# Performance work log

Measured on AMD Instinct MI355X. Metric: run time of the kernel, lower is better.

The kernel has to match this reference:

```python
import jax, jax.numpy as jnp
import numpy as np

B, S, D = 32, 2048, 1024
TEMP = 9.0  # RelaxedBernoulli temperature (torch.tensor([9]))


def setup_inputs() -> dict:
    key = jax.random.key(0)
    ks = jax.random.split(key, 12)
    sd = 1.0 / np.sqrt(D)
    sd2 = 1.0 / np.sqrt(2 * D)
    return {
        "h_t": jax.random.normal(ks[0], (B, D), jnp.float32),
        "h_s": jax.random.normal(ks[1], (B, S, D), jnp.float32),
        "auxi_hs": jax.random.normal(ks[2], (B, S, D), jnp.float32),
        "noise_u": jax.random.uniform(ks[3], (B, S, 1), jnp.float32),
        # linear_map: Linear(2*dim, 1) with bias
        "Wmap": jax.random.normal(ks[4], (2 * D,), jnp.float32) * sd2,
        "bmap": jax.random.normal(ks[5], (), jnp.float32) * sd2,
        # mlp_h: Linear(dim, dim) + Tanh + Linear(dim, 1)
        "W1": jax.random.normal(ks[6], (D, D), jnp.float32) * sd,
        "b1": jax.random.normal(ks[7], (D,), jnp.float32) * sd,
        "W2": jax.random.normal(ks[8], (D,), jnp.float32) * sd,
        "b2": jax.random.normal(ks[9], (), jnp.float32) * sd,
        # linear_out: Linear(2*dim, dim, bias=False) (attn_type='dot')
        "Wout": jax.random.normal(ks[10], (D, 2 * D), jnp.float32) * sd2,
    }


def reference(h_t, h_s, auxi_hs, noise_u, Wmap, bmap, W1, b1, W2, b2, Wout):
    # h_t: (B, D) one-step query; h_s, auxi_hs: (B, S, D)
    d = h_s.shape[-1]
    # linear_map(concat(auxi_hs, H_t)) without materializing the (B,S,2D) concat
    Wm_a, Wm_t = Wmap[:d], Wmap[d:]
    logits_p = jnp.einsum('bsd,d->bs', auxi_hs, Wm_a) + (h_t @ Wm_t)[:, None] + bmap  # (B,S)
    logits_p = logits_p[..., None]  # (B,S,1); note logit(sigmoid(x)) == x
    # RelaxedBernoulli(temp=9, probs=sigmoid(logits_p)).sample() with explicit uniform noise
    eps = 1e-7
    u = jnp.clip(noise_u, eps, 1.0 - eps)
    logistic = jnp.log(u) - jnp.log1p(-u)  # (B,S,1)
    G = jax.nn.sigmoid((logits_p + logistic) / TEMP)  # (B,S,1)
    # mlp_h(h_s): Linear -> tanh -> Linear
    e = jnp.einsum('bsd,d->bs', jnp.tanh(jnp.einsum('bsd,ed->bse', h_s, W1) + b1), W2) + b2
    e = e[..., None]  # (B,S,1)
    # custom softmax: max over dim 0 (batch!), exp, gate
    v = jnp.max(e, axis=0, keepdims=True)  # (1,S,1)
    scores = jnp.exp(e - v) * G  # (B,S,1)
    align = scores[..., 0] / jnp.sum(scores[..., 0], axis=1, keepdims=True)  # (B,S)
    c = jnp.einsum('bs,bsd->bd', align, h_s)  # (B,D)
    attn_h = jnp.tanh(jnp.concatenate([c, h_t], axis=-1) @ Wout.T)  # (B,D)
    return attn_h, align
```

## Files before the change

### kernel.cpp

```cpp
#include <hip/hip_runtime.h>
#include <hip/hip_bf16.h>
#include <math.h>

#define B_ 32
#define S_ 2048
#define D_ 1024
#define TEMP_ 9.0f

typedef __attribute__((ext_vector_type(8))) short short8;
typedef __attribute__((ext_vector_type(4))) float f32x4;
typedef __attribute__((ext_vector_type(4))) unsigned short ushort4v;

__device__ __forceinline__ unsigned short f2b(float f) {
  union { float f; unsigned int u; } v; v.f = f;
  unsigned int r = v.u;
  r += 0x7fffu + ((r >> 16) & 1u);
  return (unsigned short)(r >> 16);
}
__device__ __forceinline__ float b2f(unsigned short b) {
  union { float f; unsigned int u; } v; v.u = ((unsigned int)b) << 16;
  return v.f;
}
__device__ __forceinline__ float tanh_fast(float x) {
  float ez = __expf(2.f * x);
  return 1.f - __fdividef(2.f, ez + 1.f);
}

#define GLOAD_LDS16(g, l) \
  __builtin_amdgcn_global_load_lds((const __attribute__((address_space(1))) void*)(g), \
                                   (__attribute__((address_space(3))) void*)(l), 16, 0, 0)

__global__ void k_conv(const float* __restrict__ src, unsigned short* __restrict__ dst, int n8) {
  int i = blockIdx.x * 256 + threadIdx.x;
  if (i >= n8) return;
  const float4* g = reinterpret_cast<const float4*>(src) + (size_t)i * 2;
  float4 x0 = g[0], x1 = g[1];
  uint4 w;
  w.x = f2b(x0.x) | ((unsigned)f2b(x0.y) << 16);
  w.y = f2b(x0.z) | ((unsigned)f2b(x0.w) << 16);
  w.z = f2b(x1.x) | ((unsigned)f2b(x1.y) << 16);
  w.w = f2b(x1.z) | ((unsigned)f2b(x1.w) << 16);
  reinterpret_cast<uint4*>(dst)[i] = w;
}

__global__ void k_pack_w1(const float* __restrict__ W1, unsigned short* __restrict__ w1t) {
  int c = blockIdx.x * 256 + threadIdx.x;
  int l  = c & 63;
  int kt = (c >> 6) & 31;
  int cg = c >> 11;
  int col = cg * 16 + (l & 15);
  int k0  = kt * 32 + (l >> 4) * 8;
  const float* src = W1 + (size_t)col * D_ + k0;
  float4 x0 = *reinterpret_cast<const float4*>(src);
  float4 x1 = *reinterpret_cast<const float4*>(src + 4);
  uint4 w;
  w.x = f2b(x0.x) | ((unsigned)f2b(x0.y) << 16);
  w.y = f2b(x0.z) | ((unsigned)f2b(x0.w) << 16);
  w.z = f2b(x1.x) | ((unsigned)f2b(x1.y) << 16);
  w.w = f2b(x1.z) | ((unsigned)f2b(x1.w) << 16);
  reinterpret_cast<uint4*>(w1t)[c] = w;
}

__global__ void k0_tdot(const float* __restrict__ h_t, const float* __restrict__ Wmap,
                        const float* __restrict__ bmap, float* __restrict__ tdot) {
  int b = blockIdx.x;
  int t = threadIdx.x;
  float p = 0.f;
  for (int k = t; k < D_; k += 256) p += h_t[b*D_ + k] * Wmap[D_ + k];
  __shared__ float red[256];
  red[t] = p; __syncthreads();
  for (int off = 128; off > 0; off >>= 1) { if (t < off) red[t] += red[t+off]; __syncthreads(); }
  if (t == 0) tdot[b] = red[0] + bmap[0];
}

__global__ void k1_gate(const float* __restrict__ aux, const float* __restrict__ Wmap,
                        const float* __restrict__ noise, const float* __restrict__ tdot,
                        float* __restrict__ Gout) {
  int w = (blockIdx.x * 256 + threadIdx.x) >> 6;
  int lane = threadIdx.x & 63;
  const float4* arow = reinterpret_cast<const float4*>(aux + (size_t)w * D_);
  const float4* wrow = reinterpret_cast<const float4*>(Wmap);
  float p = 0.f;
  for (int it = 0; it < 4; ++it) {
    float4 a = arow[it*64 + lane];
    float4 m = wrow[it*64 + lane];
    p += a.x*m.x + a.y*m.y + a.z*m.z + a.w*m.w;
  }
  for (int msk = 32; msk > 0; msk >>= 1) p += __shfl_xor(p, msk);
  if (lane == 0) {
    int b = w >> 11;
    float logits = p + tdot[b];
    float u = noise[w];
    u = fminf(fmaxf(u, 1e-7f), 1.f - 1e-7f);
    float logistic = logf(u) - log1pf(-u);
    float x = (logits + logistic) / TEMP_;
    Gout[w] = 1.f / (1.f + expf(-x));
  }
}

extern __shared__ unsigned short lds2[];

__global__ __launch_bounds__(256, 2) void k2gt(
    const unsigned short* __restrict__ Ag, const unsigned short* __restrict__ w1t,
    const float* __restrict__ b1, const float* __restrict__ W2,
    float* __restrict__ e_buf,
    const float* __restrict__ aux, const float* __restrict__ Wmap,
    const float* __restrict__ noise, const float* __restrict__ tdot,
    float* __restrict__ Gout) {
  int bid = blockIdx.x;
  int xcd = bid & 7;
  int sub = bid >> 3;
  int cc  = sub & 3;
  int rc  = xcd + 8 * (sub >> 2);
  int rowBase = rc * 128;
  int colBase = cc * 256;

  int t = threadIdx.x;
  int lane = t & 63;
  int wv = t >> 6;
  int kslot = lane >> 4;

  int aOff[8];
#pragma unroll
  for (int m = 0; m < 8; ++m) {
    int r = m * 16 + (lane & 15);
    aOff[m] = r * 64 + ((kslot ^ ((r >> 1) & 3)) << 4);
  }

  const unsigned short* gA[2];
  int dstA[2];
#pragma unroll
  for (int i = 0; i < 2; ++i) {
    int c = i * 256 + t;
    int r = c >> 2;
    int clog = (c & 3) ^ ((r >> 1) & 3);
    gA[i] = Ag + (size_t)(rowBase + r) * D_ + clog * 8;
    dstA[i] = c * 16;
  }

  const unsigned short* pB[4];
#pragma unroll
  for (int n = 0; n < 4; ++n) {
    int cg = (colBase >> 4) + wv * 4 + n;
    pB[n] = w1t + (size_t)cg * 16384 + lane * 8;
  }

  f32x4 acc[8][4] = {};
  short8 bfA[4], bfB[4];

#define STAGE(TT) do {                                                         \
    char* _ba = (char*)lds2 + ((TT) & 3) * 8192;                               \
    GLOAD_LDS16(gA[0] + (TT) * 32, _ba + dstA[0]);                             \
    GLOAD_LDS16(gA[1] + (TT) * 32, _ba + dstA[1]);                             \
  } while (0)

#define K2_TILE(T, VM, DO_B, DO_S, BFC, BFN) do {                              \
    asm volatile("s_waitcnt lgkmcnt(0)\n\ts_waitcnt vmcnt(" #VM ")" ::: "memory"); \
    __builtin_amdgcn_s_barrier();                                              \
    const char* _ab = (const char*)lds2 + ((T) & 3) * 8192;                    \
    short8 af[8];                                                              \
    _Pragma("unroll")                                                          \
    for (int m = 0; m < 8; ++m)                                                \
      af[m] = *reinterpret_cast<const short8*>(_ab + aOff[m]);                 \
    if (DO_B) {                                                                \
      _Pragma("unroll")                                                        \
      for (int n = 0; n < 4; ++n)                                              \
        BFN[n] = *reinterpret_cast<const short8*>(pB[n] + ((T) + 1) * 512);    \
    }                                                                          \
    if (DO_S) STAGE((T) + 3);                                                  \
    __builtin_amdgcn_s_setprio(1);                                             \
    _Pragma("unroll")                                                          \
    for (int m = 0; m < 8; ++m)                                                \
      _Pragma("unroll")                                                        \
      for (int n = 0; n < 4; ++n)                                              \
        acc[m][n] = __builtin_amdgcn_mfma_f32_16x16x32_bf16(af[m], BFC[n], acc[m][n], 0, 0, 0); \
    __builtin_amdgcn_s_setprio(0);                                             \
  } while (0)

  STAGE(0); STAGE(1); STAGE(2);
#pragma unroll
  for (int n = 0; n < 4; ++n)
    bfA[n] = *reinterpret_cast<const short8*>(pB[n]);

  K2_TILE(0, 0, true, true, bfA, bfB);
  K2_TILE(1, 2, true, true, bfB, bfA);
#pragma unroll
  for (int tt = 2; tt < 28; tt += 2) {
    K2_TILE(tt,     2, true, true, bfA, bfB);
    K2_TILE(tt + 1, 2, true, true, bfB, bfA);
  }
  K2_TILE(28, 2, true,  true,  bfA, bfB);
  K2_TILE(29, 2, true,  false, bfB, bfA);
  K2_TILE(30, 0, true,  false, bfA, bfB);
  K2_TILE(31, 0, false, false, bfB, bfA);
#undef K2_TILE
#undef STAGE

  float b1v[4], w2v[4];
#pragma unroll
  for (int n = 0; n < 4; ++n) {
    int col = colBase + wv * 64 + n * 16 + (lane & 15);
    b1v[n] = b1[col];
    w2v[n] = W2[col];
  }
#pragma unroll
  for (int m = 0; m < 8; ++m) {
#pragma unroll
    for (int j = 0; j < 4; ++j) {
      float s = 0.f;
#pragma unroll
      for (int n = 0; n < 4; ++n)
        s += tanh_fast(acc[m][n][j] + b1v[n]) * w2v[n];
      s += __shfl_xor(s, 1);
      s += __shfl_xor(s, 2);
      s += __shfl_xor(s, 4);
      s += __shfl_xor(s, 8);
      if ((lane & 15) == 0) {
        int row = rowBase + m * 16 + ((lane >> 4) << 2) + j;
        atomicAdd(&e_buf[row], s);
      }
    }
  }

  {
    const float4* wrow = reinterpret_cast<const float4*>(Wmap);
    float4 m0 = wrow[lane], m1 = wrow[64 + lane], m2 = wrow[128 + lane], m3 = wrow[192 + lane];
    int rowG = (bid << 5) | (wv << 3);
#pragma unroll 2
    for (int i = 0; i < 8; ++i) {
      int row = rowG + i;
      const float4* arow = reinterpret_cast<const float4*>(aux + (size_t)row * D_);
      float4 a0 = arow[lane], a1 = arow[64 + lane], a2 = arow[128 + lane], a3 = arow[192 + lane];
      float p = a0.x*m0.x + a0.y*m0.y + a0.z*m0.z + a0.w*m0.w
              + a1.x*m1.x + a1.y*m1.y + a1.z*m1.z + a1.w*m1.w
              + a2.x*m2.x + a2.y*m2.y + a2.z*m2.z + a2.w*m2.w
              + a3.x*m3.x + a3.y*m3.y + a3.z*m3.z + a3.w*m3.w;
      for (int msk = 32; msk > 0; msk >>= 1) p += __shfl_xor(p, msk);
      if (lane == 0) {
        float logits = p + tdot[row >> 11];
        float u = noise[row];
        u = fminf(fmaxf(u, 1e-7f), 1.f - 1e-7f);
        float logistic = logf(u) - log1pf(-u);
        float x = (logits + logistic) / TEMP_;
        Gout[row] = 1.f / (1.f + expf(-x));
      }
    }
  }
}

#define BM 128
#define BN 128
#define BK 64
__global__ __launch_bounds__(256) void k2_egemm_f32(
    const float* __restrict__ h_s, const float* __restrict__ W1,
    const float* __restrict__ b1, const float* __restrict__ W2,
    float* __restrict__ e_buf) {
  __shared__ unsigned short As[BM * BK];
  __shared__ unsigned short Bs[BN * BK];
  int bid = blockIdx.x;
  int colBase = (bid & 7) * BN;
  int rowBase = (bid >> 3) * BM;
  int t = threadIdx.x;
  int lane = t & 63;
  int wave = t >> 6;
  int wr = wave >> 1, wc = wave & 1;
  f32x4 acc[4][4] = {};
  for (int k0 = 0; k0 < D_; k0 += BK) {
    __syncthreads();
    for (int i = 0; i < 4; ++i) {
      int flat = i*256 + t;
      int r = flat >> 3;
      int c8 = flat & 7;
      int byte = (r*128 + c8*16) ^ ((r & 7) << 4);
      {
        const float4* g = reinterpret_cast<const float4*>(h_s + (size_t)(rowBase + r)*D_ + k0 + c8*8);
        float4 x0 = g[0], x1 = g[1];
        uint4 w;
        w.x = f2b(x0.x) | ((unsigned)f2b(x0.y) << 16);
        w.y = f2b(x0.z) | ((unsigned)f2b(x0.w) << 16);
        w.z = f2b(x1.x) | ((unsigned)f2b(x1.y) << 16);
        w.w = f2b(x1.z) | ((unsigned)f2b(x1.w) << 16);
        *reinterpret_cast<uint4*>(reinterpret_cast<char*>(As) + byte) = w;
      }
      {
        const float4* g = reinterpret_cast<const float4*>(W1 + (size_t)(colBase + r)*D_ + k0 + c8*8);
        float4 x0 = g[0], x1 = g[1];
        uint4 w;
        w.x = f2b(x0.x) | ((unsigned)f2b(x0.y) << 16);
        w.y = f2b(x0.z) | ((unsigned)f2b(x0.w) << 16);
        w.z = f2b(x1.x) | ((unsigned)f2b(x1.y) << 16);
        w.w = f2b(x1.z) | ((unsigned)f2b(x1.w) << 16);
        *reinterpret_cast<uint4*>(reinterpret_cast<char*>(Bs) + byte) = w;
      }
    }
    __syncthreads();
    for (int kk = 0; kk < BK; kk += 32) {
      short8 af[4], bf[4];
      int kByte = kk*2 + ((lane >> 4) << 4);
      for (int m = 0; m < 4; ++m) {
        int r = wr*64 + m*16 + (lane & 15);
        int byte = (r*128 + kByte) ^ ((r & 7) << 4);
        af[m] = *reinterpret_cast<const short8*>(reinterpret_cast<const char*>(As) + byte);
      }
      for (int n = 0; n < 4; ++n) {
        int r = wc*64 + n*16 + (lane & 15);
        int byte = (r*128 + kByte) ^ ((r & 7) << 4);
        bf[n] = *reinterpret_cast<const short8*>(reinterpret_cast<const char*>(Bs) + byte);
      }
      for (int m = 0; m < 4; ++m)
        for (int n = 0; n < 4; ++n)
          acc[m][n] = __builtin_amdgcn_mfma_f32_16x16x32_bf16(af[m], bf[n], acc[m][n], 0, 0, 0);
    }
  }
  float b1v[4], w2v[4];
  for (int n = 0; n < 4; ++n) {
    int col = colBase + wc*64 + n*16 + (lane & 15);
    b1v[n] = b1[col];
    w2v[n] = W2[col];
  }
  for (int m = 0; m < 4; ++m) {
    for (int j = 0; j < 4; ++j) {
      float s = 0.f;
      for (int n = 0; n < 4; ++n)
        s += tanhf(acc[m][n][j] + b1v[n]) * w2v[n];
      s += __shfl_xor(s, 1);
      s += __shfl_xor(s, 2);
      s += __shfl_xor(s, 4);
      s += __shfl_xor(s, 8);
      if ((lane & 15) == 0) {
        int row = rowBase + wr*64 + m*16 + ((lane >> 4) << 2) + j;
        atomicAdd(&e_buf[row], s);
      }
    }
  }
}

__global__ void k3a_vmax(const float* __restrict__ e_buf, float* __restrict__ v) {
  int s = blockIdx.x * 256 + threadIdx.x;
  if (s >= S_) return;
  float m = -1e30f;
  for (int b = 0; b < B_; ++b) m = fmaxf(m, e_buf[b*S_ + s]);
  v[s] = m;
}

__global__ void k3b_align(const float* __restrict__ e_buf, const float* __restrict__ v,
                          float* __restrict__ galign) {
  int b = blockIdx.x;
  int t = threadIdx.x;
  __shared__ float sc[S_];
  __shared__ float red[256];
  float p = 0.f;
  for (int s = t; s < S_; s += 256) {
    float x = expf(e_buf[b*S_ + s] - v[s]) * galign[b*S_ + s];
    sc[s] = x;
    p += x;
  }
  red[t] = p; __syncthreads();
  for (int off = 128; off > 0; off >>= 1) { if (t < off) red[t] += red[t+off]; __syncthreads(); }
  float inv = 1.f / red[0];
  for (int s = t; s < S_; s += 256) galign[b*S_ + s] = sc[s] * inv;
}

__global__ void k4_ctx_bf16(const unsigned short* __restrict__ hsb, const float* __restrict__ align,
                            float* __restrict__ c) {
  int bid = blockIdx.x;
  int b = bid >> 6;
  int sBase = (bid & 63) * 32;
  int t = threadIdx.x;
  float4 accv = {0.f, 0.f, 0.f, 0.f};
  for (int si = 0; si < 32; ++si) {
    int s = sBase + si;
    float a = align[b*S_ + s];
    ushort4v hv = *reinterpret_cast<const ushort4v*>(hsb + (size_t)(b*S_ + s)*D_ + t*4);
    accv.x += a*b2f(hv.x); accv.y += a*b2f(hv.y); accv.z += a*b2f(hv.z); accv.w += a*b2f(hv.w);
  }
  atomicAdd(&c[b*D_ + t*4 + 0], accv.x);
  atomicAdd(&c[b*D_ + t*4 + 1], accv.y);
  atomicAdd(&c[b*D_ + t*4 + 2], accv.z);
  atomicAdd(&c[b*D_ + t*4 + 3], accv.w);
}

__global__ void k4_ctx_f32(const float* __restrict__ h_s, const float* __restrict__ align,
                           float* __restrict__ c) {
  int bid = blockIdx.x;
  int b = bid >> 6;
  int sBase = (bid & 63) * 32;
  int t = threadIdx.x;
  float4 accv = {0.f, 0.f, 0.f, 0.f};
  for (int si = 0; si < 32; ++si) {
    int s = sBase + si;
    float a = align[b*S_ + s];
    float4 hv = *reinterpret_cast<const float4*>(h_s + (size_t)(b*S_ + s)*D_ + t*4);
    accv.x += a*hv.x; accv.y += a*hv.y; accv.z += a*hv.z; accv.w += a*hv.w;
  }
  atomicAdd(&c[b*D_ + t*4 + 0], accv.x);
  atomicAdd(&c[b*D_ + t*4 + 1], accv.y);
  atomicAdd(&c[b*D_ + t*4 + 2], accv.z);
  atomicAdd(&c[b*D_ + t*4 + 3], accv.w);
}

__global__ void k5_out(const float* __restrict__ c, const float* __restrict__ h_t,
                       const float* __restrict__ Wout, float* __restrict__ out) {
  int W = (blockIdx.x * 256 + threadIdx.x) >> 6;
  int lane = threadIdx.x & 63;
  int b = W >> 10;
  int o = W & 1023;
  const float* wrow = Wout + (size_t)o * (2 * D_);
  float p = 0.f;
  for (int it = 0; it < 16; ++it) {
    int k = it*64 + lane;
    p += c[b*D_ + k] * wrow[k];
  }
  for (int it = 16; it < 32; ++it) {
    int k = it*64 + lane;
    p += h_t[b*D_ + (k - D_)] * wrow[k];
  }
  for (int m = 32; m > 0; m >>= 1) p += __shfl_xor(p, m);
  if (lane == 0) out[b*D_ + o] = tanhf(p);
}

extern "C" void kernel_launch(void* const* d_in, const int* in_sizes, int n_in,
                              void* d_out, int out_size, void* d_ws, size_t ws_size,
                              hipStream_t stream) {
  const float* h_t   = (const float*)d_in[0];
  const float* h_s   = (const float*)d_in[1];
  const float* aux   = (const float*)d_in[2];
  const float* noise = (const float*)d_in[3];
  const float* Wmap  = (const float*)d_in[4];
  const float* bmap  = (const float*)d_in[5];
  const float* W1    = (const float*)d_in[6];
  const float* b1    = (const float*)d_in[7];
  const float* W2    = (const float*)d_in[8];
  const float* Wout  = (const float*)d_in[10];

  float* out    = (float*)d_out;
  float* galign = out + B_*D_;

  const size_t HS_N   = (size_t)B_*S_*D_;
  const size_t W1_N   = (size_t)D_*D_;
  const size_t needed = HS_N*2 + W1_N*2 + (65536 + 32 + 2048 + 32768) * sizeof(float);

  if (ws_size >= needed) {
    unsigned short* hs_bf = (unsigned short*)d_ws;
    unsigned short* w1t   = hs_bf + HS_N;
    float* fws   = (float*)(w1t + W1_N);
    float* e_buf = fws;
    float* tdot  = fws + 65536;
    float* v     = fws + 65568;
    float* c     = fws + 67616;

    hipMemsetAsync(e_buf, 0, 65536 * sizeof(float), stream);
    hipMemsetAsync(c, 0, 32768 * sizeof(float), stream);

    hipFuncSetAttribute(reinterpret_cast<const void*>(k2gt),
                        hipFuncAttributeMaxDynamicSharedMemorySize, 32768);

    k_conv<<<(int)(HS_N/8/256), 256, 0, stream>>>(h_s, hs_bf, (int)(HS_N/8));
    k_pack_w1<<<512, 256, 0, stream>>>(W1, w1t);
    k0_tdot<<<32, 256, 0, stream>>>(h_t, Wmap, bmap, tdot);
    k2gt<<<2048, 256, 32768, stream>>>(hs_bf, w1t, b1, W2, e_buf,
                                       aux, Wmap, noise, tdot, galign);
    k3a_vmax<<<8, 256, 0, stream>>>(e_buf, v);
    k3b_align<<<32, 256, 0, stream>>>(e_buf, v, galign);
    k4_ctx_bf16<<<2048, 256, 0, stream>>>(hs_bf, galign, c);
    k5_out<<<8192, 256, 0, stream>>>(c, h_t, Wout, out);
  } else {
    float* ws    = (float*)d_ws;
    float* e_buf = ws;
    float* tdot  = ws + 65536;
    float* v     = ws + 65568;
    float* c     = ws + 67616;

    hipMemsetAsync(e_buf, 0, 65536 * sizeof(float), stream);
    hipMemsetAsync(c, 0, 32768 * sizeof(float), stream);

    k0_tdot<<<32, 256, 0, stream>>>(h_t, Wmap, bmap, tdot);
    k1_gate<<<16384, 256, 0, stream>>>(aux, Wmap, noise, tdot, galign);
    k2_egemm_f32<<<4096, 256, 0, stream>>>(h_s, W1, b1, W2, e_buf);
    k3a_vmax<<<8, 256, 0, stream>>>(e_buf, v);
    k3b_align<<<32, 256, 0, stream>>>(e_buf, v, galign);
    k4_ctx_f32<<<2048, 256, 0, stream>>>(h_s, galign, c);
    k5_out<<<8192, 256, 0, stream>>>(c, h_t, Wout, out);
  }
}
```

Measured before the change: 340.3 us.

## Remap GEMM warp tiling to 2x2 grid with 64x128 per-wave tiles

Changes the per-wave tile of the h_s·W1ᵀ MFMA GEMM from 128 rows × 64 cols to 64 rows × 128 cols, arranging the four waves as a 2×2 grid. The W1 packing kernel is reordered so each wave reads its eight B fragments for a k-step from one contiguous region. Each wave now issues half as many LDS reads for A and twice as many global loads for B per k-step. The aim is to cut LDS traffic and improve the balance of A versus B reuse, at the cost of more B register fragments and more global B bandwidth per wave.

```diff
diff --git a/kernel.cpp b/kernel.cpp
--- a/kernel.cpp
+++ b/kernel.cpp
@@ -44,12 +44,13 @@
 }
 
 __global__ void k_pack_w1(const float* __restrict__ W1, unsigned short* __restrict__ w1t) {
-  int c = blockIdx.x * 256 + threadIdx.x;
-  int l  = c & 63;
-  int kt = (c >> 6) & 31;
-  int cg = c >> 11;
-  int col = cg * 16 + (l & 15);
-  int k0  = kt * 32 + (l >> 4) * 8;
+  int c2 = blockIdx.x * 256 + threadIdx.x;
+  int l   = c2 & 63;
+  int n   = (c2 >> 6) & 7;
+  int T   = (c2 >> 9) & 31;
+  int rid = c2 >> 14;
+  int col = (rid >> 1) * 256 + (rid & 1) * 128 + n * 16 + (l & 15);
+  int k0  = T * 32 + (l >> 4) * 8;
   const float* src = W1 + (size_t)col * D_ + k0;
   float4 x0 = *reinterpret_cast<const float4*>(src);
   float4 x1 = *reinterpret_cast<const float4*>(src + 4);
@@ -58,7 +59,7 @@
   w.y = f2b(x0.z) | ((unsigned)f2b(x0.w) << 16);
   w.z = f2b(x1.x) | ((unsigned)f2b(x1.y) << 16);
   w.w = f2b(x1.z) | ((unsigned)f2b(x1.w) << 16);
-  reinterpret_cast<uint4*>(w1t)[c] = w;
+  reinterpret_cast<uint4*>(w1t)[c2] = w;
 }
 
 __global__ void k0_tdot(const float* __restrict__ h_t, const float* __restrict__ Wmap,
@@ -118,12 +119,13 @@
   int t = threadIdx.x;
   int lane = t & 63;
   int wv = t >> 6;
+  int wr = wv >> 1, wc = wv & 1;
   int kslot = lane >> 4;
 
-  int aOff[8];
-#pragma unroll
-  for (int m = 0; m < 8; ++m) {
-    int r = m * 16 + (lane & 15);
+  int aOff[4];
+#pragma unroll
+  for (int m = 0; m < 4; ++m) {
+    int r = wr * 64 + m * 16 + (lane & 15);
     aOff[m] = r * 64 + ((kslot ^ ((r >> 1) & 3)) << 4);
   }
 
@@ -138,15 +140,10 @@
     dstA[i] = c * 16;
   }
 
-  const unsigned short* pB[4];
-#pragma unroll
-  for (int n = 0; n < 4; ++n) {
-    int cg = (colBase >> 4) + wv * 4 + n;
-    pB[n] = w1t + (size_t)cg * 16384 + lane * 8;
-  }
-
-  f32x4 acc[8][4] = {};
-  short8 bfA[4], bfB[4];
+  const unsigned short* pBbase = w1t + (size_t)(cc * 2 + wc) * 131072 + lane * 8;
+
+  f32x4 acc[4][8] = {};
+  short8 bfA[8], bfB[8];
 
 #define STAGE(TT) do {                                                         \
     char* _ba = (char*)lds2 + ((TT) & 3) * 8192;                               \
@@ -158,65 +155,63 @@
     asm volatile("s_waitcnt lgkmcnt(0)\n\ts_waitcnt vmcnt(" #VM ")" ::: "memory"); \
     __builtin_amdgcn_s_barrier();                                              \
     const char* _ab = (const char*)lds2 + ((T) & 3) * 8192;                    \
-    short8 af[8];                                                              \
+    short8 af[4];                                                              \
     _Pragma("unroll")                                                          \
-    for (int m = 0; m < 8; ++m)                                                \
+    for (int m = 0; m < 4; ++m)                                                \
       af[m] = *reinterpret_cast<const short8*>(_ab + aOff[m]);                 \
     if (DO_B) {                                                                \
       _Pragma("unroll")                                                        \
-      for (int n = 0; n < 4; ++n)                                              \
-        BFN[n] = *reinterpret_cast<const short8*>(pB[n] + ((T) + 1) * 512);    \
+      for (int n = 0; n < 8; ++n)                                              \
+        BFN[n] = *reinterpret_cast<const short8*>(pBbase + ((T) + 1) * 4096 + n * 512); \
     }                                                                          \
     if (DO_S) STAGE((T) + 3);                                                  \
     __builtin_amdgcn_s_setprio(1);                                             \
     _Pragma("unroll")                                                          \
-    for (int m = 0; m < 8; ++m)                                                \
+    for (int m = 0; m < 4; ++m)                                                \
       _Pragma("unroll")                                                        \
-      for (int n = 0; n < 4; ++n)                                              \
+      for (int n = 0; n < 8; ++n)                                              \
         acc[m][n] = __builtin_amdgcn_mfma_f32_16x16x32_bf16(af[m], BFC[n], acc[m][n], 0, 0, 0); \
     __builtin_amdgcn_s_setprio(0);                                             \
   } while (0)
 
   STAGE(0); STAGE(1); STAGE(2);
 #pragma unroll
-  for (int n = 0; n < 4; ++n)
-    bfA[n] = *reinterpret_cast<const short8*>(pB[n]);
+  for (int n = 0; n < 8; ++n)
+    bfA[n] = *reinterpret_cast<const short8*>(pBbase + n * 512);
 
   K2_TILE(0, 0, true, true, bfA, bfB);
-  K2_TILE(1, 2, true, true, bfB, bfA);
-#pragma unroll
-  for (int tt = 2; tt < 28; tt += 2) {
-    K2_TILE(tt,     2, true, true, bfA, bfB);
-    K2_TILE(tt + 1, 2, true, true, bfB, bfA);
-  }
-  K2_TILE(28, 2, true,  true,  bfA, bfB);
+#pragma unroll
+  for (int tt = 1; tt < 28; tt += 2) {
+    K2_TILE(tt,     2, true, true, bfB, bfA);
+    K2_TILE(tt + 1, 2, true, true, bfA, bfB);
+  }
   K2_TILE(29, 2, true,  false, bfB, bfA);
   K2_TILE(30, 0, true,  false, bfA, bfB);
   K2_TILE(31, 0, false, false, bfB, bfA);
 #undef K2_TILE
 #undef STAGE
 
-  float b1v[4], w2v[4];
-#pragma unroll
-  for (int n = 0; n < 4; ++n) {
-    int col = colBase + wv * 64 + n * 16 + (lane & 15);
+  float b1v[8], w2v[8];
+#pragma unroll
+  for (int n = 0; n < 8; ++n) {
+    int col = colBase + wc * 128 + n * 16 + (lane & 15);
     b1v[n] = b1[col];
     w2v[n] = W2[col];
   }
 #pragma unroll
-  for (int m = 0; m < 8; ++m) {
+  for (int m = 0; m < 4; ++m) {
 #pragma unroll
     for (int j = 0; j < 4; ++j) {
       float s = 0.f;
 #pragma unroll
-      for (int n = 0; n < 4; ++n)
+      for (int n = 0; n < 8; ++n)
         s += tanh_fast(acc[m][n][j] + b1v[n]) * w2v[n];
       s += __shfl_xor(s, 1);
       s += __shfl_xor(s, 2);
       s += __shfl_xor(s, 4);
       s += __shfl_xor(s, 8);
       if ((lane & 15) == 0) {
-        int row = rowBase + m * 16 + ((lane >> 4) << 2) + j;
+        int row = rowBase + wr * 64 + m * 16 + ((lane >> 4) << 2) + j;
         atomicAdd(&e_buf[row], s);
       }
     }
```

After: 350.0 us. 1.03x slower.
